# Kernel optimization log

Measured on AMD Instinct MI355X. Metric: run time of the kernel, lower is better.

The kernel has to match this reference:

```python
import jax, jax.numpy as jnp
import numpy as np

NUM_HEADS = 8
DIM_NODE, DIM_EDGE, DIM_TIME, DIM_OUT = 512, 172, 100, 512
U_NODE, U_EDGE, U_TIME, NUM_DST, E = 100000, 8192, 50000, 16384, 131072


def _linear_params(k, fan_in, fan_out):
    # torch.nn.Linear default init: U(-1/sqrt(fan_in), 1/sqrt(fan_in))
    kw, kb = jax.random.split(k)
    bound = 1.0 / np.sqrt(fan_in)
    w = jax.random.uniform(kw, (fan_in, fan_out), jnp.float32, -bound, bound)
    b = jax.random.uniform(kb, (fan_out,), jnp.float32, -bound, bound)
    return w, b


def setup_inputs() -> dict:
    key = jax.random.key(0)
    ks = jax.random.split(key, 16)
    inp = {}
    inp["idx"] = jax.random.randint(ks[0], (E,), 0, NUM_DST, jnp.int32)
    inp["nodeData"] = jax.random.normal(ks[1], (U_NODE, DIM_NODE), jnp.float32)
    inp["node_inverse"] = jax.random.randint(ks[2], (E,), 0, U_NODE, jnp.int32)
    inp["node_dst_inverse"] = jax.random.randint(ks[3], (NUM_DST,), 0, U_NODE, jnp.int32)
    inp["efeat_unique"] = jax.random.normal(ks[4], (U_EDGE, DIM_EDGE), jnp.float32)
    inp["efeat_inverse"] = jax.random.randint(ks[5], (E,), 0, U_EDGE, jnp.int32)
    inp["time_unique"] = jax.random.normal(ks[6], (U_TIME, DIM_TIME), jnp.float32)
    inp["time_inverse"] = jax.random.randint(ks[7], (E,), 0, U_TIME, jnp.int32)
    inp["time_dst_unique"] = jax.random.normal(ks[8], (1, DIM_TIME), jnp.float32)
    inp["time_dst_inverse"] = jnp.zeros((NUM_DST,), jnp.int32)
    inp["wq_node_w"], inp["wq_node_b"] = _linear_params(ks[9], DIM_NODE, DIM_OUT)
    inp["wq_time_w"], inp["wq_time_b"] = _linear_params(ks[10], DIM_TIME, DIM_OUT)
    inp["wkv_node_w"], inp["wkv_node_b"] = _linear_params(ks[11], DIM_NODE, 2 * DIM_OUT)
    inp["wkv_edge_w"], inp["wkv_edge_b"] = _linear_params(ks[12], DIM_EDGE, 2 * DIM_OUT)
    inp["wkv_time_w"], inp["wkv_time_b"] = _linear_params(ks[13], DIM_TIME, 2 * DIM_OUT)
    return inp


def reference(idx, nodeData, node_inverse, node_dst_inverse, efeat_unique,
              efeat_inverse, time_unique, time_inverse, time_dst_unique,
              time_dst_inverse, wq_node_w, wq_node_b, wq_time_w, wq_time_b,
              wkv_node_w, wkv_node_b, wkv_edge_w, wkv_edge_b, wkv_time_w,
              wkv_time_b):
    # project on UNIQUE rows, then scatter via inverse indices (dedup pattern)
    q_node = (nodeData @ wq_node_w + wq_node_b)[node_dst_inverse]      # [num_dst, D]
    q_time = (time_dst_unique @ wq_time_w + wq_time_b)[time_dst_inverse]
    Q = (q_node + q_time)[idx]                                          # [E, D]
    z_node = (nodeData @ wkv_node_w + wkv_node_b)[node_inverse]         # [E, 2D]
    z_edge = (efeat_unique @ wkv_edge_w + wkv_edge_b)[efeat_inverse]
    z_time = (time_unique @ wkv_time_w + wkv_time_b)[time_inverse]
    Z = z_node + z_edge + z_time
    D = wq_node_w.shape[1]
    K, V = Z[:, :D], Z[:, D:]
    n = Q.shape[0]
    Qh = Q.reshape(n, NUM_HEADS, -1)
    Kh = K.reshape(n, NUM_HEADS, -1)
    Vh = V.reshape(n, NUM_HEADS, -1)
    attn = jnp.sum(Qh * Kh, axis=2)                                      # [E, H]
    attn = jnp.where(attn >= 0, attn, 0.2 * attn)                        # LeakyReLU(0.2)
    return attn, Vh
```

## Files before the change

### kernel.cpp

```cpp
#include <hip/hip_runtime.h>
#include <hip/hip_bf16.h>

typedef __bf16 bf16_t;
typedef __bf16 bf16x8 __attribute__((ext_vector_type(8)));
typedef float  f32x4  __attribute__((ext_vector_type(4)));

#define E_NUM   131072
#define NDST    16384
#define DN      512
#define DE      172
#define DEP     192
#define DT      100
#define DTP     128
#define DO      512
#define KTOT    832
#define VBASE   (E_NUM * 8)

typedef const __attribute__((address_space(1))) char gbl_t;
typedef __attribute__((address_space(3))) char lds_t;

#define GLOAD_LDS16(g, l) __builtin_amdgcn_global_load_lds((gbl_t*)(g), (lds_t*)(l), 16, 0, 0)

__global__ void cvt_bf16_vec(const float* __restrict__ src, bf16_t* __restrict__ dst, long n8) {
    long i = (long)blockIdx.x * blockDim.x + threadIdx.x;
    long stride = (long)gridDim.x * blockDim.x;
    for (; i < n8; i += stride) {
        const float4* p = reinterpret_cast<const float4*>(src + i * 8);
        float4 a = p[0], b = p[1];
        union { bf16_t h[8]; uint4 q; } t;
        t.h[0]=(bf16_t)a.x; t.h[1]=(bf16_t)a.y; t.h[2]=(bf16_t)a.z; t.h[3]=(bf16_t)a.w;
        t.h[4]=(bf16_t)b.x; t.h[5]=(bf16_t)b.y; t.h[6]=(bf16_t)b.z; t.h[7]=(bf16_t)b.w;
        *reinterpret_cast<uint4*>(dst + i * 8) = t.q;
    }
}

__global__ void cvt_pad(const float* __restrict__ src, bf16_t* __restrict__ dst,
                        int rows, int cin, int cout) {
    long total = (long)rows * cout;
    long i = (long)blockIdx.x * blockDim.x + threadIdx.x;
    long stride = (long)gridDim.x * blockDim.x;
    for (; i < total; i += stride) {
        int r = (int)(i / cout), c = (int)(i - (long)r * cout);
        dst[i] = (c < cin) ? (bf16_t)src[(size_t)r * cin + c] : (bf16_t)0.0f;
    }
}

__global__ void prep_wkvT(const float* __restrict__ wn, const float* __restrict__ we,
                          const float* __restrict__ wt, const float* __restrict__ bn,
                          const float* __restrict__ be, const float* __restrict__ bt,
                          bf16_t* __restrict__ WkvT, float* __restrict__ kvbias) {
    int n = blockIdx.x;
    for (int k = threadIdx.x; k < KTOT; k += blockDim.x) {
        float v;
        if (k < 512)            v = wn[(size_t)k * 1024 + n];
        else if (k < 512 + DE)  v = we[(size_t)(k - 512) * 1024 + n];
        else if (k < 704)       v = 0.0f;
        else if (k < 704 + DT)  v = wt[(size_t)(k - 704) * 1024 + n];
        else                    v = 0.0f;
        WkvT[(size_t)n * KTOT + k] = (bf16_t)v;
    }
    if (threadIdx.x == 0) kvbias[n] = bn[n] + be[n] + bt[n];
}

__global__ void prep_wqT(const float* __restrict__ wq, bf16_t* __restrict__ WqT) {
    int n = blockIdx.x;
    for (int k = threadIdx.x; k < DO; k += blockDim.x)
        WqT[(size_t)n * DO + k] = (bf16_t)wq[(size_t)k * DO + n];
}

__global__ void prep_qbias(const float* __restrict__ td, const float* __restrict__ wqt,
                           const float* __restrict__ bqt, const float* __restrict__ bqn,
                           float* __restrict__ qbias) {
    int n = blockIdx.x * blockDim.x + threadIdx.x;
    if (n < DO) {
        float s = bqt[n] + bqn[n];
        for (int k = 0; k < DT; ++k) s += td[k] * wqt[(size_t)k * DO + n];
        qbias[n] = s;
    }
}

__global__ __launch_bounds__(256) void qd_gemm_kernel(
    const bf16_t* __restrict__ node_bf, const int* __restrict__ node_dst,
    const bf16_t* __restrict__ WqT, const float* __restrict__ qbias,
    float* __restrict__ QD) {
    const int bx = blockIdx.x;
    const int mt = bx >> 2, nt = bx & 3;
    const int d0 = mt * 128, n0 = nt * 128;
    const int tid = threadIdx.x;
    const int lane = tid & 63, wid = tid >> 6;
    const int wm = wid >> 1, wn = wid & 1;
    const int lr = lane & 15, lg = lane >> 4;

    __shared__ __align__(16) bf16_t Ash[2][128 * 32];
    __shared__ __align__(16) bf16_t Bsh[2][128 * 32];

    const int srow = wid * 32 + (lane >> 2);
    const int achk = lane & 3;
    const bf16_t* pa0 = node_bf + (size_t)node_dst[d0 + srow] * DN + achk * 8;
    const bf16_t* pa1 = node_bf + (size_t)node_dst[d0 + srow + 16] * DN + achk * 8;
    const bf16_t* pb0 = WqT + (size_t)(n0 + srow) * DO + achk * 8;
    const bf16_t* pb1 = pb0 + (size_t)16 * DO;

#define QD_STAGE(buf, kt) do {                                                   \
        int k0_ = (kt) * 32;                                                     \
        GLOAD_LDS16(pa0 + k0_, &Ash[buf][0] + wid * 1024);                       \
        GLOAD_LDS16(pa1 + k0_, &Ash[buf][0] + wid * 1024 + 512);                 \
        GLOAD_LDS16(pb0 + k0_, &Bsh[buf][0] + wid * 1024);                       \
        GLOAD_LDS16(pb1 + k0_, &Bsh[buf][0] + wid * 1024 + 512);                 \
    } while (0)

    f32x4 acc[4][4];
#pragma unroll
    for (int i = 0; i < 4; ++i)
#pragma unroll
        for (int j = 0; j < 4; ++j) { acc[i][j][0]=0.f; acc[i][j][1]=0.f; acc[i][j][2]=0.f; acc[i][j][3]=0.f; }

    QD_STAGE(0, 0);
    __syncthreads();
    int cur = 0;
    for (int kt = 0; kt < 16; ++kt) {
        if (kt < 15) QD_STAGE(cur ^ 1, kt + 1);
        bf16x8 af[4], bfr[4];
#pragma unroll
        for (int mi = 0; mi < 4; ++mi)
            af[mi] = *reinterpret_cast<const bf16x8*>(&Ash[cur][(wm * 64 + mi * 16 + lr) * 32 + lg * 8]);
#pragma unroll
        for (int ni = 0; ni < 4; ++ni)
            bfr[ni] = *reinterpret_cast<const bf16x8*>(&Bsh[cur][(wn * 64 + ni * 16 + lr) * 32 + lg * 8]);
#pragma unroll
        for (int mi = 0; mi < 4; ++mi)
#pragma unroll
            for (int ni = 0; ni < 4; ++ni)
                acc[mi][ni] = __builtin_amdgcn_mfma_f32_16x16x32_bf16(af[mi], bfr[ni], acc[mi][ni], 0, 0, 0);
        __syncthreads();
        cur ^= 1;
    }

    float qb[4];
#pragma unroll
    for (int ni = 0; ni < 4; ++ni) qb[ni] = qbias[n0 + wn * 64 + ni * 16 + lr];
#pragma unroll
    for (int mi = 0; mi < 4; ++mi)
#pragma unroll
        for (int j = 0; j < 4; ++j) {
            int m = wm * 64 + mi * 16 + lg * 4 + j;
            float* op = QD + (size_t)(d0 + m) * DO + n0 + wn * 64 + lr;
#pragma unroll
            for (int ni = 0; ni < 4; ++ni) op[ni * 16] = acc[mi][ni][j] + qb[ni];
        }
#undef QD_STAGE
}

__global__ __launch_bounds__(512) void kv_attn_kernel(
    const bf16_t* __restrict__ node_bf, const bf16_t* __restrict__ edge_bf,
    const bf16_t* __restrict__ time_bf, const int* __restrict__ node_inverse,
    const int* __restrict__ efeat_inverse, const int* __restrict__ time_inverse,
    const int* __restrict__ idx, const bf16_t* __restrict__ WkvT,
    const float* __restrict__ kvbias, const float* __restrict__ QD,
    float* __restrict__ out) {
    const int bx = blockIdx.x;
    const int mt = bx >> 2, nt = bx & 3;
    const int e0 = mt * 128, n0 = nt * 256;
    const int tid = threadIdx.x;
    const int lane = tid & 63, wid = tid >> 6;
    const int wm = wid >> 2, wn = wid & 3;
    const int lr = lane & 15, lg = lane >> 4;

    __shared__ __align__(16) bf16_t Ash[2][128 * 32];
    __shared__ __align__(16) bf16_t Bsh[2][256 * 32];
    __shared__ int qrow_s[128];

    if (tid < 128) qrow_s[tid] = idx[e0 + tid];

    const int arow = wid * 16 + (lane >> 2);
    const int achk = lane & 3;
    const int ae = e0 + arow;
    const bf16_t* pn = node_bf + (size_t)node_inverse[ae] * DN  + achk * 8;
    const bf16_t* pe = edge_bf + (size_t)efeat_inverse[ae] * DEP + achk * 8;
    const bf16_t* pt = time_bf + (size_t)time_inverse[ae] * DTP + achk * 8;
    const int brow = wid * 32 + (lane >> 2);
    const bf16_t* pb0 = WkvT + (size_t)(n0 + brow) * KTOT + achk * 8;
    const bf16_t* pb1 = pb0 + (size_t)16 * KTOT;

#define KV_STAGE(buf, kt) do {                                                   \
        int k0_ = (kt) * 32;                                                     \
        const bf16_t* ga_;                                                       \
        if (k0_ < 512)      ga_ = pn + k0_;                                      \
        else if (k0_ < 704) ga_ = pe + (k0_ - 512);                              \
        else                ga_ = pt + (k0_ - 704);                              \
        GLOAD_LDS16(ga_,       &Ash[buf][0] + wid * 512);                        \
        GLOAD_LDS16(pb0 + k0_, &Bsh[buf][0] + wid * 1024);                       \
        GLOAD_LDS16(pb1 + k0_, &Bsh[buf][0] + wid * 1024 + 512);                 \
    } while (0)

    f32x4 acc[4][4];
#pragma unroll
    for (int i = 0; i < 4; ++i)
#pragma unroll
        for (int j = 0; j < 4; ++j) { acc[i][j][0]=0.f; acc[i][j][1]=0.f; acc[i][j][2]=0.f; acc[i][j][3]=0.f; }

    KV_STAGE(0, 0);
    __syncthreads();
    int cur = 0;
    for (int kt = 0; kt < 26; ++kt) {
        if (kt < 25) KV_STAGE(cur ^ 1, kt + 1);
        bf16x8 af[4], bfr[4];
#pragma unroll
        for (int mi = 0; mi < 4; ++mi)
            af[mi] = *reinterpret_cast<const bf16x8*>(&Ash[cur][(wm * 64 + mi * 16 + lr) * 32 + lg * 8]);
#pragma unroll
        for (int ni = 0; ni < 4; ++ni)
            bfr[ni] = *reinterpret_cast<const bf16x8*>(&Bsh[cur][(wn * 64 + ni * 16 + lr) * 32 + lg * 8]);
#pragma unroll
        for (int mi = 0; mi < 4; ++mi)
#pragma unroll
            for (int ni = 0; ni < 4; ++ni)
                acc[mi][ni] = __builtin_amdgcn_mfma_f32_16x16x32_bf16(af[mi], bfr[ni], acc[mi][ni], 0, 0, 0);
        __syncthreads();
        cur ^= 1;
    }
#undef KV_STAGE

    float kvb[4];
#pragma unroll
    for (int ni = 0; ni < 4; ++ni) kvb[ni] = kvbias[n0 + wn * 64 + ni * 16 + lr];

    if (nt < 2) {
        const int head = nt * 4 + wn;
        const int hcol = head * 64;
        float p[4][4];
#pragma unroll
        for (int mi = 0; mi < 4; ++mi)
#pragma unroll
            for (int j = 0; j < 4; ++j) {
                int m = wm * 64 + mi * 16 + lg * 4 + j;
                int qr = qrow_s[m];
                const float* qp = QD + (size_t)qr * DO + hcol + lr;
                float s = 0.f;
#pragma unroll
                for (int ni = 0; ni < 4; ++ni)
                    s += (acc[mi][ni][j] + kvb[ni]) * qp[ni * 16];
                p[mi][j] = s;
            }
#pragma unroll
        for (int off = 1; off < 16; off <<= 1)
#pragma unroll
            for (int mi = 0; mi < 4; ++mi)
#pragma unroll
                for (int j = 0; j < 4; ++j)
                    p[mi][j] += __shfl_xor(p[mi][j], off, 64);
        if (lr == 0) {
#pragma unroll
            for (int mi = 0; mi < 4; ++mi)
#pragma unroll
                for (int j = 0; j < 4; ++j) {
                    int e = e0 + wm * 64 + mi * 16 + lg * 4 + j;
                    float s = p[mi][j];
                    out[(size_t)e * 8 + head] = (s >= 0.f) ? s : 0.2f * s;
                }
        }
    } else {
        const int vcol0 = n0 - 512 + wn * 64;
#pragma unroll
        for (int mi = 0; mi < 4; ++mi)
#pragma unroll
            for (int j = 0; j < 4; ++j) {
                int e = e0 + wm * 64 + mi * 16 + lg * 4 + j;
                float* op = out + VBASE + (size_t)e * 512 + vcol0 + lr;
#pragma unroll
                for (int ni = 0; ni < 4; ++ni) op[ni * 16] = acc[mi][ni][j] + kvb[ni];
            }
    }
}

extern "C" void kernel_launch(void* const* d_in, const int* in_sizes, int n_in,
                              void* d_out, int out_size, void* d_ws, size_t ws_size,
                              hipStream_t stream) {
    const int*   idx        = (const int*)d_in[0];
    const float* nodeData   = (const float*)d_in[1];
    const int*   node_inv   = (const int*)d_in[2];
    const int*   node_dst   = (const int*)d_in[3];
    const float* efeat      = (const float*)d_in[4];
    const int*   efeat_inv  = (const int*)d_in[5];
    const float* time_u     = (const float*)d_in[6];
    const int*   time_inv   = (const int*)d_in[7];
    const float* time_dst   = (const float*)d_in[8];
    const float* wq_node_w  = (const float*)d_in[10];
    const float* wq_node_b  = (const float*)d_in[11];
    const float* wq_time_w  = (const float*)d_in[12];
    const float* wq_time_b  = (const float*)d_in[13];
    const float* wkv_node_w = (const float*)d_in[14];
    const float* wkv_node_b = (const float*)d_in[15];
    const float* wkv_edge_w = (const float*)d_in[16];
    const float* wkv_edge_b = (const float*)d_in[17];
    const float* wkv_time_w = (const float*)d_in[18];
    const float* wkv_time_b = (const float*)d_in[19];

    char* ws = (char*)d_ws;
    bf16_t* node_bf = (bf16_t*)(ws + 0);
    bf16_t* edge_bf = (bf16_t*)(ws + 102400000);
    bf16_t* time_bf = (bf16_t*)(ws + 105545728);
    bf16_t* WkvT    = (bf16_t*)(ws + 118345728);
    bf16_t* WqT     = (bf16_t*)(ws + 120049664);
    float*  kvbias  = (float*)(ws + 120573952);
    float*  qbias   = (float*)(ws + 120578048);
    float*  QD      = (float*)(ws + 120580096);
    float*  out     = (float*)d_out;

    cvt_bf16_vec<<<2048, 256, 0, stream>>>(nodeData, node_bf, (long)100000 * 512 / 8);
    cvt_pad<<<512, 256, 0, stream>>>(efeat, edge_bf, 8192, DE, DEP);
    cvt_pad<<<1024, 256, 0, stream>>>(time_u, time_bf, 50000, DT, DTP);
    prep_wkvT<<<1024, 256, 0, stream>>>(wkv_node_w, wkv_edge_w, wkv_time_w,
                                        wkv_node_b, wkv_edge_b, wkv_time_b, WkvT, kvbias);
    prep_wqT<<<512, 256, 0, stream>>>(wq_node_w, WqT);
    prep_qbias<<<2, 256, 0, stream>>>(time_dst, wq_time_w, wq_time_b, wq_node_b, qbias);
    qd_gemm_kernel<<<512, 256, 0, stream>>>(node_bf, node_dst, WqT, qbias, QD);
    kv_attn_kernel<<<4096, 512, 0, stream>>>(node_bf, edge_bf, time_bf, node_inv,
                                             efeat_inv, time_inv, idx, WkvT, kvbias, QD, out);
}
```

Baseline: 428.3 us.

## Retile KV GEMM to 256x256x64 with swizzled LDS and phased ping-pong schedule

The fused KV-projection/attention kernel now computes 256x256 output tiles with a K-step of 64 instead of 128x256 with a K-step of 32. This halves the grid and doubles data reuse per LDS load. LDS moves to 128 KB of dynamic shared memory, and an XOR swizzle on column chunks avoids bank conflicts. The main loop is split into four read/MFMA phases with explicit sched_barriers, manual vmcnt waits and setprio, so the next tile's global-to-LDS loads overlap the current MFMAs. The cost is higher register pressure and a single resident block per CU, which reduces occupancy. The hand-counted waits are also fragile.

```diff
diff --git a/kernel.cpp b/kernel.cpp
--- a/kernel.cpp
+++ b/kernel.cpp
@@ -20,6 +20,16 @@
 typedef __attribute__((address_space(3))) char lds_t;
 
 #define GLOAD_LDS16(g, l) __builtin_amdgcn_global_load_lds((gbl_t*)(g), (lds_t*)(l), 16, 0, 0)
+
+#define SBAR() do {                                  \
+        __builtin_amdgcn_sched_barrier(0);           \
+        asm volatile("" ::: "memory");               \
+        __builtin_amdgcn_s_barrier();                \
+        asm volatile("" ::: "memory");               \
+        __builtin_amdgcn_sched_barrier(0);           \
+    } while (0)
+
+#define WAITVM(n) asm volatile("s_waitcnt vmcnt(" #n ")" ::: "memory")
 
 __global__ void cvt_bf16_vec(const float* __restrict__ src, bf16_t* __restrict__ dst, long n8) {
     long i = (long)blockIdx.x * blockDim.x + threadIdx.x;
@@ -151,125 +161,213 @@
 #undef QD_STAGE
 }
 
-__global__ __launch_bounds__(512) void kv_attn_kernel(
+__global__ __launch_bounds__(512, 2) void kv_attn_kernel(
     const bf16_t* __restrict__ node_bf, const bf16_t* __restrict__ edge_bf,
     const bf16_t* __restrict__ time_bf, const int* __restrict__ node_inverse,
     const int* __restrict__ efeat_inverse, const int* __restrict__ time_inverse,
     const int* __restrict__ idx, const bf16_t* __restrict__ WkvT,
     const float* __restrict__ kvbias, const float* __restrict__ QD,
     float* __restrict__ out) {
+    extern __shared__ char smem[];
+
     const int bx = blockIdx.x;
     const int mt = bx >> 2, nt = bx & 3;
-    const int e0 = mt * 128, n0 = nt * 256;
+    const int e0 = mt * 256, n0 = nt * 256;
     const int tid = threadIdx.x;
     const int lane = tid & 63, wid = tid >> 6;
     const int wm = wid >> 2, wn = wid & 3;
     const int lr = lane & 15, lg = lane >> 4;
 
-    __shared__ __align__(16) bf16_t Ash[2][128 * 32];
-    __shared__ __align__(16) bf16_t Bsh[2][256 * 32];
-    __shared__ int qrow_s[128];
-
-    if (tid < 128) qrow_s[tid] = idx[e0 + tid];
-
-    const int arow = wid * 16 + (lane >> 2);
-    const int achk = lane & 3;
-    const int ae = e0 + arow;
-    const bf16_t* pn = node_bf + (size_t)node_inverse[ae] * DN  + achk * 8;
-    const bf16_t* pe = edge_bf + (size_t)efeat_inverse[ae] * DEP + achk * 8;
-    const bf16_t* pt = time_bf + (size_t)time_inverse[ae] * DTP + achk * 8;
-    const int brow = wid * 32 + (lane >> 2);
-    const bf16_t* pb0 = WkvT + (size_t)(n0 + brow) * KTOT + achk * 8;
-    const bf16_t* pb1 = pb0 + (size_t)16 * KTOT;
-
-#define KV_STAGE(buf, kt) do {                                                   \
-        int k0_ = (kt) * 32;                                                     \
-        const bf16_t* ga_;                                                       \
-        if (k0_ < 512)      ga_ = pn + k0_;                                      \
-        else if (k0_ < 704) ga_ = pe + (k0_ - 512);                              \
-        else                ga_ = pt + (k0_ - 704);                              \
-        GLOAD_LDS16(ga_,       &Ash[buf][0] + wid * 512);                        \
-        GLOAD_LDS16(pb0 + k0_, &Bsh[buf][0] + wid * 1024);                       \
-        GLOAD_LDS16(pb1 + k0_, &Bsh[buf][0] + wid * 1024 + 512);                 \
+    const char* nodeB = (const char*)node_bf;
+    const char* edgeB = (const char*)edge_bf;
+    const char* timeB = (const char*)time_bf;
+    const char* wkvB  = (const char*)WkvT;
+
+    const int l8 = lane >> 3, c8 = lane & 7;
+    const unsigned colb = (unsigned)((c8 ^ l8) * 16);
+
+    unsigned offN[4], offE[4], offT[4], offB[4];
+#pragma unroll
+    for (int s = 0; s < 4; ++s) {
+        int half = s >> 1, i = s & 1;
+        int r = half * 128 + wid * 16 + i * 8 + l8;
+        int e = e0 + r;
+        offN[s] = (unsigned)node_inverse[e] * 1024u + colb;
+        offE[s] = (unsigned)efeat_inverse[e] * 384u + colb;
+        offT[s] = (unsigned)time_inverse[e] * 256u + colb;
+        offB[s] = (unsigned)(n0 + r) * 1664u + colb;
+    }
+
+#define ISSUE_A(nbuf, t_, half_) do {                                             \
+        const char* sb_; unsigned so_, o0_, o1_;                                  \
+        if ((t_) < 8)       { sb_ = nodeB; so_ = (unsigned)(t_) * 128u;           \
+                              o0_ = offN[(half_)*2]; o1_ = offN[(half_)*2+1]; }   \
+        else if ((t_) < 11) { sb_ = edgeB; so_ = (unsigned)((t_)-8) * 128u;       \
+                              o0_ = offE[(half_)*2]; o1_ = offE[(half_)*2+1]; }   \
+        else                { sb_ = timeB; so_ = (unsigned)((t_)-11) * 128u;      \
+                              o0_ = offT[(half_)*2]; o1_ = offT[(half_)*2+1]; }   \
+        GLOAD_LDS16(sb_ + o0_ + so_, smem + (nbuf)*32768 + ((half_)*128 + wid*16) * 128);       \
+        GLOAD_LDS16(sb_ + o1_ + so_, smem + (nbuf)*32768 + ((half_)*128 + wid*16 + 8) * 128);   \
     } while (0)
 
-    f32x4 acc[4][4];
-#pragma unroll
-    for (int i = 0; i < 4; ++i)
-#pragma unroll
-        for (int j = 0; j < 4; ++j) { acc[i][j][0]=0.f; acc[i][j][1]=0.f; acc[i][j][2]=0.f; acc[i][j][3]=0.f; }
-
-    KV_STAGE(0, 0);
-    __syncthreads();
+#define ISSUE_B(nbuf, t_, half_) do {                                             \
+        GLOAD_LDS16(wkvB + offB[(half_)*2]   + (unsigned)(t_)*128u,               \
+                    smem + 65536 + (nbuf)*32768 + ((half_)*128 + wid*16) * 128);  \
+        GLOAD_LDS16(wkvB + offB[(half_)*2+1] + (unsigned)(t_)*128u,               \
+                    smem + 65536 + (nbuf)*32768 + ((half_)*128 + wid*16 + 8) * 128); \
+    } while (0)
+
+    const int axb0 = ((lg ^ (lr & 7)) * 16);
+    const int axb1 = (((4 + lg) ^ (lr & 7)) * 16);
+    const int aRowB = (wm * 64 + lr) * 128;
+    const int bRowB = (wn * 64 + lr) * 128;
+
+    f32x4 acc[2][4][2][2];
+#pragma unroll
+    for (int a = 0; a < 2; ++a)
+#pragma unroll
+        for (int b = 0; b < 4; ++b)
+#pragma unroll
+            for (int c = 0; c < 2; ++c)
+#pragma unroll
+                for (int d = 0; d < 2; ++d) {
+                    acc[a][b][c][d][0]=0.f; acc[a][b][c][d][1]=0.f;
+                    acc[a][b][c][d][2]=0.f; acc[a][b][c][d][3]=0.f;
+                }
+    bf16x8 aF[4][2], bF[2][2];
+
+#define PH_READ_A(mh_) do {                                                       \
+        _Pragma("unroll")                                                         \
+        for (int mi = 0; mi < 4; ++mi) {                                          \
+            const char* p_ = smem + cur*32768 + aRowB + (mh_)*16384 + mi*2048;    \
+            aF[mi][0] = *reinterpret_cast<const bf16x8*>(p_ + axb0);              \
+            aF[mi][1] = *reinterpret_cast<const bf16x8*>(p_ + axb1);              \
+        } } while (0)
+
+#define PH_READ_B(nh_) do {                                                       \
+        _Pragma("unroll")                                                         \
+        for (int nj = 0; nj < 2; ++nj) {                                          \
+            const char* p_ = smem + 65536 + cur*32768 + bRowB + (nh_)*4096 + nj*2048; \
+            bF[nj][0] = *reinterpret_cast<const bf16x8*>(p_ + axb0);              \
+            bF[nj][1] = *reinterpret_cast<const bf16x8*>(p_ + axb1);              \
+        } } while (0)
+
+#define PH_MFMA(mh_, nh_) do {                                                    \
+        __builtin_amdgcn_s_setprio(1);                                            \
+        _Pragma("unroll")                                                         \
+        for (int mi = 0; mi < 4; ++mi)                                            \
+        _Pragma("unroll")                                                         \
+        for (int nj = 0; nj < 2; ++nj) {                                          \
+            acc[mh_][mi][nh_][nj] = __builtin_amdgcn_mfma_f32_16x16x32_bf16(      \
+                aF[mi][0], bF[nj][0], acc[mh_][mi][nh_][nj], 0, 0, 0);            \
+            acc[mh_][mi][nh_][nj] = __builtin_amdgcn_mfma_f32_16x16x32_bf16(      \
+                aF[mi][1], bF[nj][1], acc[mh_][mi][nh_][nj], 0, 0, 0);            \
+        }                                                                         \
+        __builtin_amdgcn_s_setprio(0); } while (0)
+
+    ISSUE_A(0, 0, 0); ISSUE_B(0, 0, 0); ISSUE_B(0, 0, 1); ISSUE_A(0, 0, 1);
+    WAITVM(2);
+    SBAR();
+
     int cur = 0;
-    for (int kt = 0; kt < 26; ++kt) {
-        if (kt < 25) KV_STAGE(cur ^ 1, kt + 1);
-        bf16x8 af[4], bfr[4];
-#pragma unroll
-        for (int mi = 0; mi < 4; ++mi)
-            af[mi] = *reinterpret_cast<const bf16x8*>(&Ash[cur][(wm * 64 + mi * 16 + lr) * 32 + lg * 8]);
-#pragma unroll
-        for (int ni = 0; ni < 4; ++ni)
-            bfr[ni] = *reinterpret_cast<const bf16x8*>(&Bsh[cur][(wn * 64 + ni * 16 + lr) * 32 + lg * 8]);
-#pragma unroll
-        for (int mi = 0; mi < 4; ++mi)
-#pragma unroll
-            for (int ni = 0; ni < 4; ++ni)
-                acc[mi][ni] = __builtin_amdgcn_mfma_f32_16x16x32_bf16(af[mi], bfr[ni], acc[mi][ni], 0, 0, 0);
-        __syncthreads();
-        cur ^= 1;
-    }
-#undef KV_STAGE
-
-    float kvb[4];
-#pragma unroll
-    for (int ni = 0; ni < 4; ++ni) kvb[ni] = kvbias[n0 + wn * 64 + ni * 16 + lr];
+    for (int t = 0; t < 12; ++t) {
+        const int nb = cur ^ 1;
+        PH_READ_A(0); PH_READ_B(0);
+        ISSUE_A(nb, t + 1, 0);
+        SBAR();
+        PH_MFMA(0, 0);
+        SBAR();
+        PH_READ_B(1);
+        ISSUE_B(nb, t + 1, 0);
+        SBAR();
+        PH_MFMA(0, 1);
+        WAITVM(4);
+        SBAR();
+        PH_READ_A(1);
+        ISSUE_B(nb, t + 1, 1);
+        SBAR();
+        PH_MFMA(1, 1);
+        SBAR();
+        PH_READ_B(0);
+        ISSUE_A(nb, t + 1, 1);
+        SBAR();
+        PH_MFMA(1, 0);
+        WAITVM(2);
+        SBAR();
+        cur = nb;
+    }
+    PH_READ_A(0); PH_READ_B(0);
+    SBAR();
+    PH_MFMA(0, 0);
+    SBAR();
+    PH_READ_B(1);
+    SBAR();
+    PH_MFMA(0, 1);
+    WAITVM(0);
+    SBAR();
+    PH_READ_A(1);
+    SBAR();
+    PH_MFMA(1, 1);
+    SBAR();
+    PH_READ_B(0);
+    SBAR();
+    PH_MFMA(1, 0);
+
+#undef PH_READ_A
+#undef PH_READ_B
+#undef PH_MFMA
+#undef ISSUE_A
+#undef ISSUE_B
+
+    float kvb[2][2];
+#pragma unroll
+    for (int nh = 0; nh < 2; ++nh)
+#pragma unroll
+        for (int nj = 0; nj < 2; ++nj)
+            kvb[nh][nj] = kvbias[n0 + wn * 64 + nh * 32 + nj * 16 + lr];
 
     if (nt < 2) {
         const int head = nt * 4 + wn;
-        const int hcol = head * 64;
-        float p[4][4];
-#pragma unroll
-        for (int mi = 0; mi < 4; ++mi)
-#pragma unroll
-            for (int j = 0; j < 4; ++j) {
-                int m = wm * 64 + mi * 16 + lg * 4 + j;
-                int qr = qrow_s[m];
-                const float* qp = QD + (size_t)qr * DO + hcol + lr;
-                float s = 0.f;
-#pragma unroll
-                for (int ni = 0; ni < 4; ++ni)
-                    s += (acc[mi][ni][j] + kvb[ni]) * qp[ni * 16];
-                p[mi][j] = s;
-            }
-#pragma unroll
-        for (int off = 1; off < 16; off <<= 1)
+        const float* qbase = QD + head * 64 + lr;
+#pragma unroll
+        for (int mh = 0; mh < 2; ++mh)
 #pragma unroll
             for (int mi = 0; mi < 4; ++mi)
 #pragma unroll
-                for (int j = 0; j < 4; ++j)
-                    p[mi][j] += __shfl_xor(p[mi][j], off, 64);
-        if (lr == 0) {
+                for (int j = 0; j < 4; ++j) {
+                    int m = mh * 128 + wm * 64 + mi * 16 + lg * 4 + j;
+                    int qr = idx[e0 + m];
+                    const float* qp = qbase + (size_t)qr * DO;
+                    float s = 0.f;
+#pragma unroll
+                    for (int nh = 0; nh < 2; ++nh)
+#pragma unroll
+                        for (int nj = 0; nj < 2; ++nj)
+                            s += (acc[mh][mi][nh][nj][j] + kvb[nh][nj]) * qp[nh * 32 + nj * 16];
+                    s += __shfl_xor(s, 1, 64);
+                    s += __shfl_xor(s, 2, 64);
+                    s += __shfl_xor(s, 4, 64);
+                    s += __shfl_xor(s, 8, 64);
+                    if (lr == 0) {
+                        int e = e0 + m;
+                        out[(size_t)e * 8 + head] = (s >= 0.f) ? s : 0.2f * s;
+                    }
+                }
+    } else {
+        float* vb = out + VBASE + (nt - 2) * 256 + wn * 64 + lr;
+#pragma unroll
+        for (int mh = 0; mh < 2; ++mh)
 #pragma unroll
             for (int mi = 0; mi < 4; ++mi)
 #pragma unroll
                 for (int j = 0; j < 4; ++j) {
-                    int e = e0 + wm * 64 + mi * 16 + lg * 4 + j;
-                    float s = p[mi][j];
-                    out[(size_t)e * 8 + head] = (s >= 0.f) ? s : 0.2f * s;
+                    int m = mh * 128 + wm * 64 + mi * 16 + lg * 4 + j;
+                    float* op = vb + (size_t)(e0 + m) * 512;
+                    op[0]  = acc[mh][mi][0][0][j] + kvb[0][0];
+                    op[16] = acc[mh][mi][0][1][j] + kvb[0][1];
+                    op[32] = acc[mh][mi][1][0][j] + kvb[1][0];
+                    op[48] = acc[mh][mi][1][1][j] + kvb[1][1];
                 }
-        }
-    } else {
-        const int vcol0 = n0 - 512 + wn * 64;
-#pragma unroll
-        for (int mi = 0; mi < 4; ++mi)
-#pragma unroll
-            for (int j = 0; j < 4; ++j) {
-                int e = e0 + wm * 64 + mi * 16 + lg * 4 + j;
-                float* op = out + VBASE + (size_t)e * 512 + vcol0 + lr;
-#pragma unroll
-                for (int ni = 0; ni < 4; ++ni) op[ni * 16] = acc[mi][ni][j] + kvb[ni];
-            }
     }
 }
 
@@ -307,6 +405,9 @@
     float*  QD      = (float*)(ws + 120580096);
     float*  out     = (float*)d_out;
 
+    hipFuncSetAttribute(reinterpret_cast<const void*>(kv_attn_kernel),
+                        hipFuncAttributeMaxDynamicSharedMemorySize, 131072);
+
     cvt_bf16_vec<<<2048, 256, 0, stream>>>(nodeData, node_bf, (long)100000 * 512 / 8);
     cvt_pad<<<512, 256, 0, stream>>>(efeat, edge_bf, 8192, DE, DEP);
     cvt_pad<<<1024, 256, 0, stream>>>(time_u, time_bf, 50000, DT, DTP);
@@ -315,6 +416,6 @@
     prep_wqT<<<512, 256, 0, stream>>>(wq_node_w, WqT);
     prep_qbias<<<2, 256, 0, stream>>>(time_dst, wq_time_w, wq_time_b, wq_node_b, qbias);
     qd_gemm_kernel<<<512, 256, 0, stream>>>(node_bf, node_dst, WqT, qbias, QD);
-    kv_attn_kernel<<<4096, 512, 0, stream>>>(node_bf, edge_bf, time_bf, node_inv,
-                                             efeat_inv, time_inv, idx, WkvT, kvbias, QD, out);
-}
+    kv_attn_kernel<<<2048, 512, 131072, stream>>>(node_bf, edge_bf, time_bf, node_inv,
+                                                  efeat_inv, time_inv, idx, WkvT, kvbias, QD, out);
+}
```

Result: slower. 498.4 us (+16.4%).

## Rework KV gather-GEMM into 256-row tiles with triple-buffered swizzled LDS pipeline

Applied to the files above, without the earlier changes.

Doubles the edge tile to 256 rows per block, which halves the grid and doubles how often each loaded weight tile is reused. Replaces the double-buffered loop with a three-stage LDS ring in dynamic shared memory, XOR-swizzled layout, explicit vmcnt/lgkmcnt waits, raw barriers and raised MFMA priority, so the indexed gathers overlap compute. The epilogue reads idx straight from global memory and reduces per row with shuffles, freeing registers for the doubled accumulator. In exchange it uses 96KB of LDS per block and roughly twice the accumulator registers, which may limit occupancy, and the hand-placed waits are fragile.

```diff
diff --git a/kernel.cpp b/kernel.cpp
--- a/kernel.cpp
+++ b/kernel.cpp
@@ -14,12 +14,27 @@
 #define DTP     128
 #define DO      512
 #define KTOT    832
+#define NKT     26
 #define VBASE   (E_NUM * 8)
 
 typedef const __attribute__((address_space(1))) char gbl_t;
 typedef __attribute__((address_space(3))) char lds_t;
 
 #define GLOAD_LDS16(g, l) __builtin_amdgcn_global_load_lds((gbl_t*)(g), (lds_t*)(l), 16, 0, 0)
+
+#define SBAR() do {                                  \
+        __builtin_amdgcn_sched_barrier(0);           \
+        asm volatile("" ::: "memory");               \
+        __builtin_amdgcn_s_barrier();                \
+        asm volatile("" ::: "memory");               \
+        __builtin_amdgcn_sched_barrier(0);           \
+    } while (0)
+
+#define WAITVM(n) asm volatile("s_waitcnt vmcnt(" #n ")" ::: "memory")
+#define LGKM0() do {                                             \
+        asm volatile("s_waitcnt lgkmcnt(0)" ::: "memory");       \
+        __builtin_amdgcn_sched_barrier(0);                       \
+    } while (0)
 
 __global__ void cvt_bf16_vec(const float* __restrict__ src, bf16_t* __restrict__ dst, long n8) {
     long i = (long)blockIdx.x * blockDim.x + threadIdx.x;
@@ -151,75 +166,115 @@
 #undef QD_STAGE
 }
 
-__global__ __launch_bounds__(512) void kv_attn_kernel(
+__global__ __launch_bounds__(512, 2) void kv_attn_kernel(
     const bf16_t* __restrict__ node_bf, const bf16_t* __restrict__ edge_bf,
     const bf16_t* __restrict__ time_bf, const int* __restrict__ node_inverse,
     const int* __restrict__ efeat_inverse, const int* __restrict__ time_inverse,
     const int* __restrict__ idx, const bf16_t* __restrict__ WkvT,
     const float* __restrict__ kvbias, const float* __restrict__ QD,
     float* __restrict__ out) {
+    extern __shared__ char smem[];
+
     const int bx = blockIdx.x;
     const int mt = bx >> 2, nt = bx & 3;
-    const int e0 = mt * 128, n0 = nt * 256;
+    const int e0 = mt * 256, n0 = nt * 256;
     const int tid = threadIdx.x;
     const int lane = tid & 63, wid = tid >> 6;
     const int wm = wid >> 2, wn = wid & 3;
     const int lr = lane & 15, lg = lane >> 4;
 
-    __shared__ __align__(16) bf16_t Ash[2][128 * 32];
-    __shared__ __align__(16) bf16_t Bsh[2][256 * 32];
-    __shared__ int qrow_s[128];
-
-    if (tid < 128) qrow_s[tid] = idx[e0 + tid];
-
-    const int arow = wid * 16 + (lane >> 2);
-    const int achk = lane & 3;
-    const int ae = e0 + arow;
-    const bf16_t* pn = node_bf + (size_t)node_inverse[ae] * DN  + achk * 8;
-    const bf16_t* pe = edge_bf + (size_t)efeat_inverse[ae] * DEP + achk * 8;
-    const bf16_t* pt = time_bf + (size_t)time_inverse[ae] * DTP + achk * 8;
-    const int brow = wid * 32 + (lane >> 2);
-    const bf16_t* pb0 = WkvT + (size_t)(n0 + brow) * KTOT + achk * 8;
-    const bf16_t* pb1 = pb0 + (size_t)16 * KTOT;
-
-#define KV_STAGE(buf, kt) do {                                                   \
-        int k0_ = (kt) * 32;                                                     \
-        const bf16_t* ga_;                                                       \
-        if (k0_ < 512)      ga_ = pn + k0_;                                      \
-        else if (k0_ < 704) ga_ = pe + (k0_ - 512);                              \
-        else                ga_ = pt + (k0_ - 704);                              \
-        GLOAD_LDS16(ga_,       &Ash[buf][0] + wid * 512);                        \
-        GLOAD_LDS16(pb0 + k0_, &Bsh[buf][0] + wid * 1024);                       \
-        GLOAD_LDS16(pb1 + k0_, &Bsh[buf][0] + wid * 1024 + 512);                 \
-    } while (0)
-
-    f32x4 acc[4][4];
-#pragma unroll
-    for (int i = 0; i < 4; ++i)
-#pragma unroll
-        for (int j = 0; j < 4; ++j) { acc[i][j][0]=0.f; acc[i][j][1]=0.f; acc[i][j][2]=0.f; acc[i][j][3]=0.f; }
-
-    KV_STAGE(0, 0);
-    __syncthreads();
+    const char* nodeB = (const char*)node_bf;
+    const char* edgeB = (const char*)edge_bf;
+    const char* timeB = (const char*)time_bf;
+    const char* wkvB  = (const char*)WkvT;
+
+    const int srl = lane >> 2;
+    const unsigned clog = (unsigned)(((lane & 3) ^ (srl & 3)) * 16);
+    unsigned offN[2], offE[2], offT[2], offB[2];
+#pragma unroll
+    for (int i = 0; i < 2; ++i) {
+        int r = wid * 32 + i * 16 + srl;
+        int e = e0 + r;
+        offN[i] = (unsigned)node_inverse[e]  * 1024u + clog;
+        offE[i] = (unsigned)efeat_inverse[e] * 384u  + clog;
+        offT[i] = (unsigned)time_inverse[e]  * 256u  + clog;
+        offB[i] = (unsigned)(n0 + r)         * 1664u + clog;
+    }
+    const int ldsA = wid * 2048;
+    const int ldsB = 16384 + wid * 2048;
+
+#define STAGE(i_, ts_, nb_) do {                                                  \
+        const char* ga_;                                                          \
+        if ((ts_) < 16)      ga_ = nodeB + offN[i_] + (unsigned)(ts_) * 64u;      \
+        else if ((ts_) < 22) ga_ = edgeB + offE[i_] + (unsigned)((ts_) - 16) * 64u; \
+        else                 ga_ = timeB + offT[i_] + (unsigned)((ts_) - 22) * 64u; \
+        GLOAD_LDS16(ga_, smem + (nb_) * 32768 + ldsA + (i_) * 1024);              \
+        GLOAD_LDS16(wkvB + offB[i_] + (unsigned)(ts_) * 64u,                      \
+                    smem + (nb_) * 32768 + ldsB + (i_) * 1024);                   \
+    } while (0)
+
+    const int xorb = (lg ^ (lr & 3)) * 16;
+    const int aoff = (wm * 128 + lr) * 64 + xorb;
+    const int boff = 16384 + (wn * 64 + lr) * 64 + xorb;
+
+    f32x4 acc[8][4];
+#pragma unroll
+    for (int mi = 0; mi < 8; ++mi)
+#pragma unroll
+        for (int ni = 0; ni < 4; ++ni) {
+            acc[mi][ni][0]=0.f; acc[mi][ni][1]=0.f; acc[mi][ni][2]=0.f; acc[mi][ni][3]=0.f;
+        }
+    bf16x8 aF[4], bF[4];
+
+#define READ_A(base_, mh_) do { _Pragma("unroll")                                 \
+        for (int mi = 0; mi < 4; ++mi)                                            \
+            aF[mi] = *reinterpret_cast<const bf16x8*>((base_) + aoff + ((mh_)*4 + mi) * 1024); \
+    } while (0)
+#define READ_B(base_) do { _Pragma("unroll")                                      \
+        for (int ni = 0; ni < 4; ++ni)                                            \
+            bF[ni] = *reinterpret_cast<const bf16x8*>((base_) + boff + ni * 1024); \
+    } while (0)
+#define MFMA_Q(mh_) do {                                                          \
+        __builtin_amdgcn_s_setprio(1);                                            \
+        _Pragma("unroll")                                                         \
+        for (int mi = 0; mi < 4; ++mi)                                            \
+        _Pragma("unroll")                                                         \
+        for (int ni = 0; ni < 4; ++ni)                                            \
+            acc[(mh_)*4 + mi][ni] = __builtin_amdgcn_mfma_f32_16x16x32_bf16(      \
+                aF[mi], bF[ni], acc[(mh_)*4 + mi][ni], 0, 0, 0);                  \
+        __builtin_amdgcn_s_setprio(0);                                            \
+    } while (0)
+
+    STAGE(0, 0, 0); STAGE(1, 0, 0);
+    STAGE(0, 1, 1); STAGE(1, 1, 1);
+    WAITVM(4);
+    SBAR();
+
     int cur = 0;
-    for (int kt = 0; kt < 26; ++kt) {
-        if (kt < 25) KV_STAGE(cur ^ 1, kt + 1);
-        bf16x8 af[4], bfr[4];
-#pragma unroll
-        for (int mi = 0; mi < 4; ++mi)
-            af[mi] = *reinterpret_cast<const bf16x8*>(&Ash[cur][(wm * 64 + mi * 16 + lr) * 32 + lg * 8]);
-#pragma unroll
-        for (int ni = 0; ni < 4; ++ni)
-            bfr[ni] = *reinterpret_cast<const bf16x8*>(&Bsh[cur][(wn * 64 + ni * 16 + lr) * 32 + lg * 8]);
-#pragma unroll
-        for (int mi = 0; mi < 4; ++mi)
-#pragma unroll
-            for (int ni = 0; ni < 4; ++ni)
-                acc[mi][ni] = __builtin_amdgcn_mfma_f32_16x16x32_bf16(af[mi], bfr[ni], acc[mi][ni], 0, 0, 0);
-        __syncthreads();
-        cur ^= 1;
-    }
-#undef KV_STAGE
+#pragma unroll 1
+    for (int t = 0; t < NKT; ++t) {
+        const int nb = (cur >= 1) ? cur - 1 : cur + 2;
+        const int ts = (t + 2 < NKT) ? t + 2 : NKT - 1;
+        const char* bufc = smem + cur * 32768;
+        READ_A(bufc, 0); READ_B(bufc);
+        STAGE(0, ts, nb);
+        SBAR();
+        LGKM0();
+        MFMA_Q(0);
+        SBAR();
+        READ_A(bufc, 1);
+        STAGE(1, ts, nb);
+        WAITVM(4);
+        SBAR();
+        LGKM0();
+        MFMA_Q(1);
+        SBAR();
+        cur = (cur == 2) ? 0 : cur + 1;
+    }
+#undef STAGE
+#undef READ_A
+#undef READ_B
+#undef MFMA_Q
 
     float kvb[4];
 #pragma unroll
@@ -227,48 +282,39 @@
 
     if (nt < 2) {
         const int head = nt * 4 + wn;
-        const int hcol = head * 64;
-        float p[4][4];
-#pragma unroll
-        for (int mi = 0; mi < 4; ++mi)
+        const float* qbase = QD + head * 64 + lr;
+#pragma unroll
+        for (int mi = 0; mi < 8; ++mi)
 #pragma unroll
             for (int j = 0; j < 4; ++j) {
-                int m = wm * 64 + mi * 16 + lg * 4 + j;
-                int qr = qrow_s[m];
-                const float* qp = QD + (size_t)qr * DO + hcol + lr;
+                int m = wm * 128 + mi * 16 + lg * 4 + j;
+                int qr = idx[e0 + m];
+                const float* qp = qbase + (size_t)qr * DO;
                 float s = 0.f;
 #pragma unroll
                 for (int ni = 0; ni < 4; ++ni)
                     s += (acc[mi][ni][j] + kvb[ni]) * qp[ni * 16];
-                p[mi][j] = s;
-            }
-#pragma unroll
-        for (int off = 1; off < 16; off <<= 1)
-#pragma unroll
-            for (int mi = 0; mi < 4; ++mi)
-#pragma unroll
-                for (int j = 0; j < 4; ++j)
-                    p[mi][j] += __shfl_xor(p[mi][j], off, 64);
-        if (lr == 0) {
-#pragma unroll
-            for (int mi = 0; mi < 4; ++mi)
-#pragma unroll
-                for (int j = 0; j < 4; ++j) {
-                    int e = e0 + wm * 64 + mi * 16 + lg * 4 + j;
-                    float s = p[mi][j];
+                s += __shfl_xor(s, 1, 64);
+                s += __shfl_xor(s, 2, 64);
+                s += __shfl_xor(s, 4, 64);
+                s += __shfl_xor(s, 8, 64);
+                if (lr == 0) {
+                    int e = e0 + m;
                     out[(size_t)e * 8 + head] = (s >= 0.f) ? s : 0.2f * s;
                 }
-        }
+            }
     } else {
-        const int vcol0 = n0 - 512 + wn * 64;
-#pragma unroll
-        for (int mi = 0; mi < 4; ++mi)
+        float* vb = out + VBASE + (nt - 2) * 256 + wn * 64 + lr;
+#pragma unroll
+        for (int mi = 0; mi < 8; ++mi)
 #pragma unroll
             for (int j = 0; j < 4; ++j) {
-                int e = e0 + wm * 64 + mi * 16 + lg * 4 + j;
-                float* op = out + VBASE + (size_t)e * 512 + vcol0 + lr;
-#pragma unroll
-                for (int ni = 0; ni < 4; ++ni) op[ni * 16] = acc[mi][ni][j] + kvb[ni];
+                int m = wm * 128 + mi * 16 + lg * 4 + j;
+                float* op = vb + (size_t)(e0 + m) * 512;
+                op[0]  = acc[mi][0][j] + kvb[0];
+                op[16] = acc[mi][1][j] + kvb[1];
+                op[32] = acc[mi][2][j] + kvb[2];
+                op[48] = acc[mi][3][j] + kvb[3];
             }
     }
 }
@@ -307,6 +353,9 @@
     float*  QD      = (float*)(ws + 120580096);
     float*  out     = (float*)d_out;
 
+    hipFuncSetAttribute(reinterpret_cast<const void*>(kv_attn_kernel),
+                        hipFuncAttributeMaxDynamicSharedMemorySize, 98304);
+
     cvt_bf16_vec<<<2048, 256, 0, stream>>>(nodeData, node_bf, (long)100000 * 512 / 8);
     cvt_pad<<<512, 256, 0, stream>>>(efeat, edge_bf, 8192, DE, DEP);
     cvt_pad<<<1024, 256, 0, stream>>>(time_u, time_bf, 50000, DT, DTP);
@@ -315,6 +364,6 @@
     prep_wqT<<<512, 256, 0, stream>>>(wq_node_w, WqT);
     prep_qbias<<<2, 256, 0, stream>>>(time_dst, wq_time_w, wq_time_b, wq_node_b, qbias);
     qd_gemm_kernel<<<512, 256, 0, stream>>>(node_bf, node_dst, WqT, qbias, QD);
-    kv_attn_kernel<<<4096, 512, 0, stream>>>(node_bf, edge_bf, time_bf, node_inv,
-                                             efeat_inv, time_inv, idx, WkvT, kvbias, QD, out);
-}
+    kv_attn_kernel<<<2048, 512, 98304, stream>>>(node_bf, edge_bf, time_bf, node_inv,
+                                                 efeat_inv, time_inv, idx, WkvT, kvbias, QD, out);
+}
```

After: 529.4 us. 23.6% more time.

## Triple-buffer GEMM pipelines with LDS swizzle, block remap and MFMA priority

Applied to the files above, without the earlier changes.

Both the Q and KV GEMM kernels move from double to triple LDS buffering. Prefetch runs two stages ahead, synchronised with explicit vmcnt waits and a raw s_barrier instead of __syncthreads. The 16-byte chunk placement within each LDS row is rotated on the global side and undone on the read side, aiming to reduce LDS bank conflicts. Block indices are remapped so neighbouring workgroups are spread out, which may change L2/cache locality. The MFMA sections are bracketed with s_setprio. The costs are more LDS per block, which may lower occupancy, and fragile hand-written waitcnt counts.

```diff
diff --git a/kernel.cpp b/kernel.cpp
--- a/kernel.cpp
+++ b/kernel.cpp
@@ -20,6 +20,16 @@
 typedef __attribute__((address_space(3))) char lds_t;
 
 #define GLOAD_LDS16(g, l) __builtin_amdgcn_global_load_lds((gbl_t*)(g), (lds_t*)(l), 16, 0, 0)
+
+#define SBAR() do {                                  \
+        __builtin_amdgcn_sched_barrier(0);           \
+        asm volatile("" ::: "memory");               \
+        __builtin_amdgcn_s_barrier();                \
+        asm volatile("" ::: "memory");               \
+        __builtin_amdgcn_sched_barrier(0);           \
+    } while (0)
+
+#define WAITVM(n) asm volatile("s_waitcnt vmcnt(" #n ")" ::: "memory")
 
 __global__ void cvt_bf16_vec(const float* __restrict__ src, bf16_t* __restrict__ dst, long n8) {
     long i = (long)blockIdx.x * blockDim.x + threadIdx.x;
@@ -83,7 +93,7 @@
     const bf16_t* __restrict__ node_bf, const int* __restrict__ node_dst,
     const bf16_t* __restrict__ WqT, const float* __restrict__ qbias,
     float* __restrict__ QD) {
-    const int bx = blockIdx.x;
+    const int bx = ((blockIdx.x & 7) << 6) + (blockIdx.x >> 3);
     const int mt = bx >> 2, nt = bx & 3;
     const int d0 = mt * 128, n0 = nt * 128;
     const int tid = threadIdx.x;
@@ -91,14 +101,14 @@
     const int wm = wid >> 1, wn = wid & 1;
     const int lr = lane & 15, lg = lane >> 4;
 
-    __shared__ __align__(16) bf16_t Ash[2][128 * 32];
-    __shared__ __align__(16) bf16_t Bsh[2][128 * 32];
+    __shared__ __align__(16) bf16_t Ash[3][128 * 32];
+    __shared__ __align__(16) bf16_t Bsh[3][128 * 32];
 
     const int srow = wid * 32 + (lane >> 2);
-    const int achk = lane & 3;
-    const bf16_t* pa0 = node_bf + (size_t)node_dst[d0 + srow] * DN + achk * 8;
-    const bf16_t* pa1 = node_bf + (size_t)node_dst[d0 + srow + 16] * DN + achk * 8;
-    const bf16_t* pb0 = WqT + (size_t)(n0 + srow) * DO + achk * 8;
+    const int csrc = ((lane & 3) - ((lane >> 3) & 3)) & 3;
+    const bf16_t* pa0 = node_bf + (size_t)node_dst[d0 + srow] * DN + csrc * 8;
+    const bf16_t* pa1 = node_bf + (size_t)node_dst[d0 + srow + 16] * DN + csrc * 8;
+    const bf16_t* pb0 = WqT + (size_t)(n0 + srow) * DO + csrc * 8;
     const bf16_t* pb1 = pb0 + (size_t)16 * DO;
 
 #define QD_STAGE(buf, kt) do {                                                   \
@@ -115,26 +125,46 @@
 #pragma unroll
         for (int j = 0; j < 4; ++j) { acc[i][j][0]=0.f; acc[i][j][1]=0.f; acc[i][j][2]=0.f; acc[i][j][3]=0.f; }
 
+    const int rchk = ((lg + (lr >> 1)) & 3) * 8;
+
+#define QD_COMPUTE(buf_) do {                                                     \
+        bf16x8 af[4], bfr[4];                                                     \
+        _Pragma("unroll")                                                         \
+        for (int mi = 0; mi < 4; ++mi)                                            \
+            af[mi] = *reinterpret_cast<const bf16x8*>(&Ash[buf_][(wm * 64 + mi * 16 + lr) * 32 + rchk]); \
+        _Pragma("unroll")                                                         \
+        for (int ni = 0; ni < 4; ++ni)                                            \
+            bfr[ni] = *reinterpret_cast<const bf16x8*>(&Bsh[buf_][(wn * 64 + ni * 16 + lr) * 32 + rchk]); \
+        __builtin_amdgcn_s_setprio(1);                                            \
+        _Pragma("unroll")                                                         \
+        for (int mi = 0; mi < 4; ++mi)                                            \
+        _Pragma("unroll")                                                         \
+        for (int ni = 0; ni < 4; ++ni)                                            \
+            acc[mi][ni] = __builtin_amdgcn_mfma_f32_16x16x32_bf16(af[mi], bfr[ni], acc[mi][ni], 0, 0, 0); \
+        __builtin_amdgcn_s_setprio(0);                                            \
+    } while (0)
+
     QD_STAGE(0, 0);
-    __syncthreads();
+    QD_STAGE(1, 1);
+    WAITVM(4);
+    SBAR();
+
     int cur = 0;
-    for (int kt = 0; kt < 16; ++kt) {
-        if (kt < 15) QD_STAGE(cur ^ 1, kt + 1);
-        bf16x8 af[4], bfr[4];
-#pragma unroll
-        for (int mi = 0; mi < 4; ++mi)
-            af[mi] = *reinterpret_cast<const bf16x8*>(&Ash[cur][(wm * 64 + mi * 16 + lr) * 32 + lg * 8]);
-#pragma unroll
-        for (int ni = 0; ni < 4; ++ni)
-            bfr[ni] = *reinterpret_cast<const bf16x8*>(&Bsh[cur][(wn * 64 + ni * 16 + lr) * 32 + lg * 8]);
-#pragma unroll
-        for (int mi = 0; mi < 4; ++mi)
-#pragma unroll
-            for (int ni = 0; ni < 4; ++ni)
-                acc[mi][ni] = __builtin_amdgcn_mfma_f32_16x16x32_bf16(af[mi], bfr[ni], acc[mi][ni], 0, 0, 0);
-        __syncthreads();
-        cur ^= 1;
-    }
+    for (int kt = 0; kt < 14; ++kt) {
+        const int nb = (cur == 0) ? 2 : cur - 1;
+        QD_STAGE(nb, kt + 2);
+        QD_COMPUTE(cur);
+        WAITVM(4);
+        SBAR();
+        cur = (cur == 2) ? 0 : cur + 1;
+    }
+    QD_COMPUTE(cur);
+    WAITVM(0);
+    SBAR();
+    cur = (cur == 2) ? 0 : cur + 1;
+    QD_COMPUTE(cur);
+#undef QD_STAGE
+#undef QD_COMPUTE
 
     float qb[4];
 #pragma unroll
@@ -148,7 +178,6 @@
 #pragma unroll
             for (int ni = 0; ni < 4; ++ni) op[ni * 16] = acc[mi][ni][j] + qb[ni];
         }
-#undef QD_STAGE
 }
 
 __global__ __launch_bounds__(512) void kv_attn_kernel(
@@ -158,7 +187,7 @@
     const int* __restrict__ idx, const bf16_t* __restrict__ WkvT,
     const float* __restrict__ kvbias, const float* __restrict__ QD,
     float* __restrict__ out) {
-    const int bx = blockIdx.x;
+    const int bx = ((blockIdx.x & 7) << 9) + (blockIdx.x >> 3);
     const int mt = bx >> 2, nt = bx & 3;
     const int e0 = mt * 128, n0 = nt * 256;
     const int tid = threadIdx.x;
@@ -166,20 +195,20 @@
     const int wm = wid >> 2, wn = wid & 3;
     const int lr = lane & 15, lg = lane >> 4;
 
-    __shared__ __align__(16) bf16_t Ash[2][128 * 32];
-    __shared__ __align__(16) bf16_t Bsh[2][256 * 32];
+    __shared__ __align__(16) bf16_t Ash[3][128 * 32];
+    __shared__ __align__(16) bf16_t Bsh[3][256 * 32];
     __shared__ int qrow_s[128];
 
     if (tid < 128) qrow_s[tid] = idx[e0 + tid];
 
+    const int csrc = ((lane & 3) - ((lane >> 3) & 3)) & 3;
     const int arow = wid * 16 + (lane >> 2);
-    const int achk = lane & 3;
     const int ae = e0 + arow;
-    const bf16_t* pn = node_bf + (size_t)node_inverse[ae] * DN  + achk * 8;
-    const bf16_t* pe = edge_bf + (size_t)efeat_inverse[ae] * DEP + achk * 8;
-    const bf16_t* pt = time_bf + (size_t)time_inverse[ae] * DTP + achk * 8;
+    const bf16_t* pn = node_bf + (size_t)node_inverse[ae] * DN  + csrc * 8;
+    const bf16_t* pe = edge_bf + (size_t)efeat_inverse[ae] * DEP + csrc * 8;
+    const bf16_t* pt = time_bf + (size_t)time_inverse[ae] * DTP + csrc * 8;
     const int brow = wid * 32 + (lane >> 2);
-    const bf16_t* pb0 = WkvT + (size_t)(n0 + brow) * KTOT + achk * 8;
+    const bf16_t* pb0 = WkvT + (size_t)(n0 + brow) * KTOT + csrc * 8;
     const bf16_t* pb1 = pb0 + (size_t)16 * KTOT;
 
 #define KV_STAGE(buf, kt) do {                                                   \
@@ -199,27 +228,46 @@
 #pragma unroll
         for (int j = 0; j < 4; ++j) { acc[i][j][0]=0.f; acc[i][j][1]=0.f; acc[i][j][2]=0.f; acc[i][j][3]=0.f; }
 
+    const int rchk = ((lg + (lr >> 1)) & 3) * 8;
+
+#define KV_COMPUTE(buf_) do {                                                     \
+        bf16x8 af[4], bfr[4];                                                     \
+        _Pragma("unroll")                                                         \
+        for (int mi = 0; mi < 4; ++mi)                                            \
+            af[mi] = *reinterpret_cast<const bf16x8*>(&Ash[buf_][(wm * 64 + mi * 16 + lr) * 32 + rchk]); \
+        _Pragma("unroll")                                                         \
+        for (int ni = 0; ni < 4; ++ni)                                            \
+            bfr[ni] = *reinterpret_cast<const bf16x8*>(&Bsh[buf_][(wn * 64 + ni * 16 + lr) * 32 + rchk]); \
+        __builtin_amdgcn_s_setprio(1);                                            \
+        _Pragma("unroll")                                                         \
+        for (int mi = 0; mi < 4; ++mi)                                            \
+        _Pragma("unroll")                                                         \
+        for (int ni = 0; ni < 4; ++ni)                                            \
+            acc[mi][ni] = __builtin_amdgcn_mfma_f32_16x16x32_bf16(af[mi], bfr[ni], acc[mi][ni], 0, 0, 0); \
+        __builtin_amdgcn_s_setprio(0);                                            \
+    } while (0)
+
     KV_STAGE(0, 0);
-    __syncthreads();
+    KV_STAGE(1, 1);
+    WAITVM(3);
+    SBAR();
+
     int cur = 0;
-    for (int kt = 0; kt < 26; ++kt) {
-        if (kt < 25) KV_STAGE(cur ^ 1, kt + 1);
-        bf16x8 af[4], bfr[4];
-#pragma unroll
-        for (int mi = 0; mi < 4; ++mi)
-            af[mi] = *reinterpret_cast<const bf16x8*>(&Ash[cur][(wm * 64 + mi * 16 + lr) * 32 + lg * 8]);
-#pragma unroll
-        for (int ni = 0; ni < 4; ++ni)
-            bfr[ni] = *reinterpret_cast<const bf16x8*>(&Bsh[cur][(wn * 64 + ni * 16 + lr) * 32 + lg * 8]);
-#pragma unroll
-        for (int mi = 0; mi < 4; ++mi)
-#pragma unroll
-            for (int ni = 0; ni < 4; ++ni)
-                acc[mi][ni] = __builtin_amdgcn_mfma_f32_16x16x32_bf16(af[mi], bfr[ni], acc[mi][ni], 0, 0, 0);
-        __syncthreads();
-        cur ^= 1;
-    }
+    for (int kt = 0; kt < 24; ++kt) {
+        const int nb = (cur == 0) ? 2 : cur - 1;
+        KV_STAGE(nb, kt + 2);
+        KV_COMPUTE(cur);
+        WAITVM(3);
+        SBAR();
+        cur = (cur == 2) ? 0 : cur + 1;
+    }
+    KV_COMPUTE(cur);
+    WAITVM(0);
+    SBAR();
+    cur = (cur == 2) ? 0 : cur + 1;
+    KV_COMPUTE(cur);
 #undef KV_STAGE
+#undef KV_COMPUTE
 
     float kvb[4];
 #pragma unroll
```

Result: slower. 547.7 us (+27.9%).
